# Performance work log

Measured on AMD Instinct MI355X. Metric: run time of the kernel, lower is better.

## Reference

```python
import jax, jax.numpy as jnp
import numpy as np

N = 50000      # nodes
E = 800000     # edges (before self-loops)
IN = 128       # in_channels
HID = 16       # hidden_channels
HEADS = 8
OUT = 16       # out_channels
NEG_SLOPE = 0.2
BN_EPS = 1e-5
LN_EPS = 1e-5


def setup_inputs() -> dict:
    key = jax.random.key(0)
    ks = jax.random.split(key, 16)
    s = 0.05
    inp = {
        "x": jax.random.normal(ks[0], (N, IN), jnp.float32),
        "edge_index": jax.random.randint(ks[1], (2, E), 0, N, jnp.int64),
        # conv1 (in=IN, out=HID, heads=HEADS, concat=True)
        "Wl1": jax.random.normal(ks[2], (HEADS * HID, IN), jnp.float32) * s,
        "bl1": jnp.zeros((HEADS * HID,), jnp.float32),
        "Wr1": jax.random.normal(ks[3], (HEADS * HID, IN), jnp.float32) * s,
        "br1": jnp.zeros((HEADS * HID,), jnp.float32),
        "att1": jax.random.normal(ks[4], (HEADS, HID), jnp.float32) * s,
        "bias1": jnp.zeros((HEADS * HID,), jnp.float32),
        # batchnorm (eval mode, running stats)
        "bn_w": jnp.ones((HEADS * HID,), jnp.float32),
        "bn_b": jnp.zeros((HEADS * HID,), jnp.float32),
        "bn_rm": jnp.zeros((HEADS * HID,), jnp.float32),
        "bn_rv": jnp.ones((HEADS * HID,), jnp.float32),
        # conv2 (in=HEADS*HID, out=OUT, heads=HEADS, concat=False)
        "Wl2": jax.random.normal(ks[5], (HEADS * OUT, HEADS * HID), jnp.float32) * s,
        "bl2": jnp.zeros((HEADS * OUT,), jnp.float32),
        "Wr2": jax.random.normal(ks[6], (HEADS * OUT, HEADS * HID), jnp.float32) * s,
        "br2": jnp.zeros((HEADS * OUT,), jnp.float32),
        "att2": jax.random.normal(ks[7], (HEADS, OUT), jnp.float32) * s,
        "bias2": jnp.zeros((OUT,), jnp.float32),
        # skip + layernorm
        "Wskip": jax.random.normal(ks[8], (OUT, IN), jnp.float32) * s,
        "ln_w": jnp.ones((OUT,), jnp.float32),
        "ln_b": jnp.zeros((OUT,), jnp.float32),
    }
    return inp


def _gatv2(x, src, dst, Wl, bl, Wr, br, att, bias, heads, ch, concat):
    """PyG GATv2Conv (share_weights=False), eval mode (no dropout)."""
    n = x.shape[0]
    xl = (x @ Wl.T + bl).reshape(n, heads, ch)   # source transform
    xr = (x @ Wr.T + br).reshape(n, heads, ch)   # target transform
    # edge-wise attention score
    e = jax.nn.leaky_relu(xl[src] + xr[dst], NEG_SLOPE)          # [E',H,C]
    score = jnp.einsum('ehc,hc->eh', e, att)                      # [E',H]
    # segment softmax over incoming edges per destination node
    smax = jax.ops.segment_max(score, dst, num_segments=n)
    ex = jnp.exp(score - smax[dst])
    denom = jax.ops.segment_sum(ex, dst, num_segments=n)
    alpha = ex / denom[dst]                                       # [E',H]
    out = jax.ops.segment_sum(alpha[:, :, None] * xl[src], dst, num_segments=n)
    if concat:
        out = out.reshape(n, heads * ch)
    else:
        out = out.mean(axis=1)
    return out + bias


def reference(x, edge_index, Wl1, bl1, Wr1, br1, att1, bias1,
              bn_w, bn_b, bn_rm, bn_rv,
              Wl2, bl2, Wr2, br2, att2, bias2,
              Wskip, ln_w, ln_b):
    n = x.shape[0]
    loops = jnp.arange(n, dtype=edge_index.dtype)
    src = jnp.concatenate([edge_index[0], loops])
    dst = jnp.concatenate([edge_index[1], loops])

    x_res = x @ Wskip.T                                            # [N,OUT]

    h = _gatv2(x, src, dst, Wl1, bl1, Wr1, br1, att1, bias1, HEADS, HID, True)
    # BatchNorm1d in eval mode
    h = (h - bn_rm) * jax.lax.rsqrt(bn_rv + BN_EPS) * bn_w + bn_b
    h = jax.nn.elu(h)

    h = _gatv2(h, src, dst, Wl2, bl2, Wr2, br2, att2, bias2, HEADS, OUT, False)

    y = h + x_res
    mu = y.mean(axis=-1, keepdims=True)
    var = ((y - mu) ** 2).mean(axis=-1, keepdims=True)
    return (y - mu) * jax.lax.rsqrt(var + LN_EPS) * ln_w + ln_b
```

## Files before the change

kernel.cpp:

```cpp
#include <hip/hip_runtime.h>

#define NEG_SLOPE 0.2f
#define BN_EPS 1e-5f
#define LN_EPS 1e-5f

#if __has_builtin(__builtin_amdgcn_exp2f)
#define EXP2F(x) __builtin_amdgcn_exp2f(x)
#else
#define EXP2F(x) exp2f(x)
#endif

typedef __bf16 bf16_t;
typedef bf16_t bf16x8 __attribute__((ext_vector_type(8)));
typedef float floatx4 __attribute__((ext_vector_type(4)));

__device__ __forceinline__ unsigned short f2bf(float f) {
  unsigned u = __float_as_uint(f);
  u += 0x7FFFu + ((u >> 16) & 1u);
  return (unsigned short)(u >> 16);
}
__device__ __forceinline__ float bf_lo(unsigned u) { return __uint_as_float(u << 16); }
__device__ __forceinline__ float bf_hi(unsigned u) { return __uint_as_float(u & 0xFFFF0000u); }

__global__ void cvt_all(const float* __restrict__ x,
                        const float* __restrict__ wl1, const float* __restrict__ wr1,
                        const float* __restrict__ wl2, const float* __restrict__ wr2,
                        const float* __restrict__ wsk,
                        const float* __restrict__ bias1,
                        const float* __restrict__ bn_w, const float* __restrict__ bn_b,
                        const float* __restrict__ bn_rm, const float* __restrict__ bn_rv,
                        const int* __restrict__ ei, int E,
                        unsigned short* __restrict__ xbf,
                        unsigned short* __restrict__ wcat1,
                        unsigned short* __restrict__ wcat2,
                        int* __restrict__ deg8, unsigned short* __restrict__ rpos,
                        float* __restrict__ bnS, float* __restrict__ bnT,
                        int n4x, int N) {
  const int W4 = 128 * 128 / 4;
  const int S4 = 16 * 128 / 4;
  int i = blockIdx.x * blockDim.x + threadIdx.x;
  const float* src;
  unsigned short* dst;
  int j;
  if (i < n4x) { src = x; dst = xbf; j = i; }
  else {
    j = i - n4x;
    if (j < W4)               { src = wl1; dst = wcat1; }
    else if (j < 2 * W4)      { src = wr1; dst = wcat1 + 128 * 128; j -= W4; }
    else if (j < 3 * W4)      { src = wl2; dst = wcat2; j -= 2 * W4; }
    else if (j < 4 * W4)      { src = wr2; dst = wcat2 + 128 * 128; j -= 3 * W4; }
    else if (j < 4 * W4 + S4) { src = wsk; dst = wcat1 + 256 * 128; j -= 4 * W4; }
    else {
      j -= 4 * W4 + S4;
      if (j < 32) {
        for (int t = j * 4; t < j * 4 + 4; ++t) {
          float S = bn_w[t] * rsqrtf(bn_rv[t] + BN_EPS);
          bnS[t] = S;
          bnT[t] = (bias1[t] - bn_rm[t]) * S + bn_b[t];
        }
      } else {
        int e = j - 32;
        if (e < E) {
          int d = ei[E + e];
          int c = (int)(blockIdx.x & 7);
          rpos[e] = (unsigned short)atomicAdd(&deg8[(size_t)c * N + d], 1);
        }
      }
      return;
    }
  }
  float4 v = ((const float4*)src)[j];
  ushort4 o;
  o.x = f2bf(v.x); o.y = f2bf(v.y); o.z = f2bf(v.z); o.w = f2bf(v.w);
  ((ushort4*)dst)[j] = o;
}

__global__ __launch_bounds__(1024)
void csr_scan(const int* __restrict__ deg8, int* __restrict__ meta,
              int* __restrict__ cbase8, int* bsum, int N) {
  __shared__ int wsum[16];
  __shared__ int sh_base;
  int b = blockIdx.x;
  int tid = threadIdx.x;
  int lane = tid & 63, wid = tid >> 6;
  int i0 = b * 4096 + tid * 4;

  int4 v[8];
#pragma unroll
  for (int c = 0; c < 8; ++c) {
    const int* p = deg8 + (size_t)c * N;
    v[c] = make_int4(0, 0, 0, 0);
    if (i0 + 3 < N) v[c] = *(const int4*)(p + i0);
    else if (i0 < N) {
      v[c].x = p[i0];
      if (i0 + 1 < N) v[c].y = p[i0 + 1];
      if (i0 + 2 < N) v[c].z = p[i0 + 2];
    }
  }
  int4 run = make_int4(0, 0, 0, 0);
#pragma unroll
  for (int c = 0; c < 8; ++c) {
    int4 t = v[c];
    v[c] = run;
    run.x += t.x; run.y += t.y; run.z += t.z; run.w += t.w;
  }
  int g1 = (run.x + 1) & ~1, g2 = (run.y + 1) & ~1, g3 = (run.z + 1) & ~1, g4 = (run.w + 1) & ~1;
  int s1 = g1, s2 = s1 + g2, s3 = s2 + g3, s4 = s3 + g4;
  int s = s4;
#pragma unroll
  for (int d = 1; d < 64; d <<= 1) { int t = __shfl_up(s, d, 64); if (lane >= d) s += t; }
  if (lane == 63) wsum[wid] = s;
  __syncthreads();
  if (tid < 16) {
    int ws = wsum[tid];
#pragma unroll
    for (int d = 1; d < 16; d <<= 1) { int t = __shfl_up(ws, d, 16); if (tid >= d) ws += t; }
    wsum[tid] = ws;
  }
  __syncthreads();
  if (tid == 0) {
    __hip_atomic_store(&bsum[b], wsum[15] + 1, __ATOMIC_RELEASE, __HIP_MEMORY_SCOPE_AGENT);
    int base = 0;
    for (int j = 0; j < b; ++j) {
      int x;
      do { x = __hip_atomic_load(&bsum[j], __ATOMIC_ACQUIRE, __HIP_MEMORY_SCOPE_AGENT); } while (x == 0);
      base += x - 1;
    }
    sh_base = base;
  }
  __syncthreads();
  int off = sh_base + (wid ? wsum[wid - 1] : 0) + (s - s4);
  int st[4] = {off, off + s1, off + s2, off + s3};
  int tv[4] = {run.x, run.y, run.z, run.w};
#pragma unroll
  for (int k = 0; k < 4; ++k)
    if (i0 + k < N) ((int2*)meta)[i0 + k] = make_int2(st[k], tv[k]);
#pragma unroll
  for (int c = 0; c < 8; ++c) {
    int* p = cbase8 + (size_t)c * N;
    if (i0 + 3 < N) {
      *(int4*)(p + i0) = make_int4(st[0] + v[c].x, st[1] + v[c].y, st[2] + v[c].z, st[3] + v[c].w);
    } else if (i0 < N) {
      p[i0] = st[0] + v[c].x;
      if (i0 + 1 < N) p[i0 + 1] = st[1] + v[c].y;
      if (i0 + 2 < N) p[i0 + 2] = st[2] + v[c].z;
    }
  }
}

__global__ void scatter_edges(const int* __restrict__ ei, int E, int ebase,
                              const int* __restrict__ cbase8,
                              const unsigned short* __restrict__ rpos,
                              unsigned short* __restrict__ csr, int N) {
  int e = blockIdx.x * blockDim.x + threadIdx.x;
  if (e < E) {
    int d = ei[E + e];
    int c = ((ebase + e) >> 8) & 7;
    csr[cbase8[(size_t)c * N + d] + (int)rpos[e]] = (unsigned short)ei[e];
  }
}

template <bool MIXED>
__global__ __launch_bounds__(256)
void gemm_bf16_mfma(const unsigned short* __restrict__ A, const unsigned short* __restrict__ B,
                    const float* __restrict__ bias0, const float* __restrict__ bias1,
                    unsigned short* __restrict__ Cbf, float* __restrict__ Cf,
                    int M, int pstrips) {
  int wave = (int)((blockIdx.x * blockDim.x + threadIdx.x) >> 6);
  int lane = threadIdx.x & 63;
  int mtiles = (M + 31) >> 5;
  if (wave >= mtiles * pstrips) return;
  int mt = wave % mtiles, ps = wave / mtiles;
  int r = lane & 15, quad = lane >> 4;

  const unsigned short* Abase = A + (size_t)(mt * 32 + r) * 128 + quad * 8;
  bf16x8 a0[4], a1[4];
#pragma unroll
  for (int k = 0; k < 4; ++k) {
    a0[k] = *(const bf16x8*)(Abase + 32 * k);
    a1[k] = *(const bf16x8*)(Abase + 16 * 128 + 32 * k);
  }

  int row0 = mt * 32 + quad * 4;
  const int Ptot = MIXED ? 272 : 256;
#pragma unroll
  for (int pp = 0; pp < 4; ++pp) {
    int p0 = ps * 64 + pp * 16;
    if (p0 >= Ptot) break;
    const unsigned short* Bbase = B + (size_t)(p0 + r) * 128 + quad * 8;
    bf16x8 b[4];
#pragma unroll
    for (int k = 0; k < 4; ++k) b[k] = *(const bf16x8*)(Bbase + 32 * k);
    floatx4 acc0 = {0.f, 0.f, 0.f, 0.f};
    floatx4 acc1 = {0.f, 0.f, 0.f, 0.f};
#pragma unroll
    for (int k = 0; k < 4; ++k) {
      acc0 = __builtin_amdgcn_mfma_f32_16x16x32_bf16(a0[k], b[k], acc0, 0, 0, 0);
      acc1 = __builtin_amdgcn_mfma_f32_16x16x32_bf16(a1[k], b[k], acc1, 0, 0, 0);
    }
    int col = p0 + r;
    if (MIXED && col >= 256) {
#pragma unroll
      for (int i = 0; i < 4; ++i) {
        if (row0 + i < M)      Cf[(size_t)(row0 + i) * 16 + (col - 256)] = acc0[i];
        if (row0 + 16 + i < M) Cf[(size_t)(row0 + 16 + i) * 16 + (col - 256)] = acc1[i];
      }
    } else {
      float bs = (col < 128) ? bias0[col] : bias1[col - 128];
#pragma unroll
      for (int i = 0; i < 4; ++i) {
        if (row0 + i < M)      Cbf[(size_t)(row0 + i) * 256 + col] = f2bf(acc0[i] + bs);
        if (row0 + 16 + i < M) Cbf[(size_t)(row0 + 16 + i) * 256 + col] = f2bf(acc1[i] + bs);
      }
    }
  }
}

template <int LAYER>
__global__ __launch_bounds__(256)
void gat_agg(const unsigned int* __restrict__ xlr,
             const int* __restrict__ meta,
             const unsigned short* __restrict__ csr,
             const float* __restrict__ att,
             const float* __restrict__ p0, const float* __restrict__ p1,
             const float* __restrict__ p2, const float* __restrict__ p3,
             void* __restrict__ outp, int n, int nwaves) {
  int lane = threadIdx.x & 63;
  int gw = (int)((blockIdx.x * blockDim.x + threadIdx.x) >> 6);
  int half = lane >> 5, sl = lane & 31;
  float4 at = ((const float4*)att)[sl];
  const float SC = 0.6f * 1.44269504f;
  float a0 = SC * at.x, a1 = SC * at.y, a2 = SC * at.z, a3 = SC * at.w;

  for (int dst = gw; dst < n; dst += nwaves) {
    int dsts = __builtin_amdgcn_readfirstlane(dst);
    int2 m = *(const int2*)(meta + 2 * (size_t)dsts);
    int beg = __builtin_amdgcn_readfirstlane(m.x);
    int dg  = __builtin_amdgcn_readfirstlane(m.y);
    const unsigned* cp = (const unsigned*)csr + (beg >> 1);

    uint2 ur = *(const uint2*)(xlr + (size_t)dsts * 128 + 64 + sl * 2);
    float xr0 = bf_lo(ur.x), xr1 = bf_hi(ur.x), xr2 = bf_lo(ur.y), xr3 = bf_hi(ur.y);
    float lA = 0.f, lB = 0.f;
    float cA0 = 0.f, cA1 = 0.f, cA2 = 0.f, cA3 = 0.f;
    float cB0 = 0.f, cB1 = 0.f, cB2 = 0.f, cB3 = 0.f;

    auto body = [&](uint2 u, float vm, bool useB, bool masked) {
      float x0 = bf_lo(u.x), x1 = bf_hi(u.x), x2 = bf_lo(u.y), x3 = bf_hi(u.y);
      float e0 = x0 + xr0, e1 = x1 + xr1, e2 = x2 + xr2, e3 = x3 + xr3;
      float sc = fmaf(fmaf(fabsf(e0), 0.66666667f, e0), a0,
                 fmaf(fmaf(fabsf(e1), 0.66666667f, e1), a1,
                 fmaf(fmaf(fabsf(e2), 0.66666667f, e2), a2,
                      fmaf(fabsf(e3), 0.66666667f, e3) * a3)));
      sc += __shfl_xor(sc, 1);
      sc += __shfl_xor(sc, 2);
      float pw = EXP2F(sc);
      if (masked) pw *= vm;
      if (useB) {
        lB += pw;
        cB0 = fmaf(pw, x0, cB0); cB1 = fmaf(pw, x1, cB1);
        cB2 = fmaf(pw, x2, cB2); cB3 = fmaf(pw, x3, cB3);
      } else {
        lA += pw;
        cA0 = fmaf(pw, x0, cA0); cA1 = fmaf(pw, x1, cA1);
        cA2 = fmaf(pw, x2, cA2); cA3 = fmaf(pw, x3, cA3);
      }
    };

    int npm = dg >> 1;
    int p = 0;
    int npm8 = npm & ~7;
    for (; p < npm8; p += 8) {
      uint2 u[8];
#pragma unroll
      for (int k = 0; k < 8; ++k) {
        unsigned pr = cp[p + k];
        int s = half ? (int)(pr >> 16) : (int)(pr & 0xFFFFu);
        u[k] = *(const uint2*)(xlr + ((size_t)s << 7) + sl * 2);
      }
#pragma unroll
      for (int k = 0; k < 8; ++k) body(u[k], 1.f, k & 1, false);
    }
    if (npm - p >= 4) {
      uint2 u[4];
#pragma unroll
      for (int k = 0; k < 4; ++k) {
        unsigned pr = cp[p + k];
        int s = half ? (int)(pr >> 16) : (int)(pr & 0xFFFFu);
        u[k] = *(const uint2*)(xlr + ((size_t)s << 7) + sl * 2);
      }
#pragma unroll
      for (int k = 0; k < 4; ++k) body(u[k], 1.f, k & 1, false);
      p += 4;
    }
    {
      int tot = dg + 1;
      uint2 u[4];
      float vm[4];
#pragma unroll
      for (int k = 0; k < 4; ++k) {
        unsigned pr = cp[p + k];
        int e0 = 2 * (p + k), e1 = e0 + 1;
        int sA = (e0 < dg) ? (int)(pr & 0xFFFFu) : dsts;
        int sB = (e1 < dg) ? (int)(pr >> 16) : dsts;
        float mA = (e0 < tot) ? 1.f : 0.f;
        float mB = (e1 < tot) ? 1.f : 0.f;
        int s = half ? sB : sA;
        vm[k] = half ? mB : mA;
        u[k] = *(const uint2*)(xlr + ((size_t)s << 7) + sl * 2);
      }
#pragma unroll
      for (int k = 0; k < 4; ++k) body(u[k], vm[k], k & 1, true);
    }

    float l = lA + lB;
    float c0 = cA0 + cB0, c1 = cA1 + cB1, c2 = cA2 + cB2, c3 = cA3 + cB3;
    l  += __shfl_xor(l, 32);
    c0 += __shfl_xor(c0, 32); c1 += __shfl_xor(c1, 32);
    c2 += __shfl_xor(c2, 32); c3 += __shfl_xor(c3, 32);
    float inv = 1.f / l;

    if (LAYER == 1) {
      float4 S = ((const float4*)p0)[sl];
      float4 T = ((const float4*)p1)[sl];
      float o0 = fmaf(c0 * inv, S.x, T.x);
      float o1 = fmaf(c1 * inv, S.y, T.y);
      float o2 = fmaf(c2 * inv, S.z, T.z);
      float o3 = fmaf(c3 * inv, S.w, T.w);
      o0 = (o0 > 0.f) ? o0 : (__expf(o0) - 1.f);
      o1 = (o1 > 0.f) ? o1 : (__expf(o1) - 1.f);
      o2 = (o2 > 0.f) ? o2 : (__expf(o2) - 1.f);
      o3 = (o3 > 0.f) ? o3 : (__expf(o3) - 1.f);
      if (half == 0) {
        uint2 o;
        o.x = ((unsigned)f2bf(o1) << 16) | f2bf(o0);
        o.y = ((unsigned)f2bf(o3) << 16) | f2bf(o2);
        ((uint2*)outp)[(size_t)dst * 32 + sl] = o;
      }
    } else {
      float y0 = c0 * inv, y1 = c1 * inv, y2 = c2 * inv, y3 = c3 * inv;
#pragma unroll
      for (int d = 4; d <= 16; d <<= 1) {
        y0 += __shfl_xor(y0, d); y1 += __shfl_xor(y1, d);
        y2 += __shfl_xor(y2, d); y3 += __shfl_xor(y3, d);
      }
      int chh = (sl & 3) * 4;
      float4 b2 = *(const float4*)(p1 + chh);
      float4 xs = *(const float4*)(p0 + (size_t)dst * 16 + chh);
      y0 = y0 * 0.125f + b2.x + xs.x;
      y1 = y1 * 0.125f + b2.y + xs.y;
      y2 = y2 * 0.125f + b2.z + xs.z;
      y3 = y3 * 0.125f + b2.w + xs.w;
      float t = (y0 + y1) + (y2 + y3);
      t += __shfl_xor(t, 1); t += __shfl_xor(t, 2);
      float mu = t * (1.f / 16.f);
      float d0 = y0 - mu, d1 = y1 - mu, d2 = y2 - mu, d3 = y3 - mu;
      float v = (d0 * d0 + d1 * d1) + (d2 * d2 + d3 * d3);
      v += __shfl_xor(v, 1); v += __shfl_xor(v, 2);
      float istd = rsqrtf(v * (1.f / 16.f) + LN_EPS);
      float4 lw = *(const float4*)(p2 + chh);
      float4 lb = *(const float4*)(p3 + chh);
      if (lane < 4) {
        float4 o;
        o.x = d0 * istd * lw.x + lb.x;
        o.y = d1 * istd * lw.y + lb.y;
        o.z = d2 * istd * lw.z + lb.z;
        o.w = d3 * istd * lw.w + lb.w;
        *(float4*)((float*)outp + (size_t)dst * 16 + chh) = o;
      }
    }
  }
}

extern "C" void kernel_launch(void* const* d_in, const int* in_sizes, int n_in,
                              void* d_out, int out_size, void* d_ws, size_t ws_size,
                              hipStream_t stream) {
  const float* x     = (const float*)d_in[0];
  const int*   ei    = (const int*)d_in[1];
  const float* Wl1   = (const float*)d_in[2];
  const float* bl1   = (const float*)d_in[3];
  const float* Wr1   = (const float*)d_in[4];
  const float* br1   = (const float*)d_in[5];
  const float* att1  = (const float*)d_in[6];
  const float* bias1 = (const float*)d_in[7];
  const float* bn_w  = (const float*)d_in[8];
  const float* bn_b  = (const float*)d_in[9];
  const float* bn_rm = (const float*)d_in[10];
  const float* bn_rv = (const float*)d_in[11];
  const float* Wl2   = (const float*)d_in[12];
  const float* bl2   = (const float*)d_in[13];
  const float* Wr2   = (const float*)d_in[14];
  const float* br2   = (const float*)d_in[15];
  const float* att2  = (const float*)d_in[16];
  const float* bias2 = (const float*)d_in[17];
  const float* Wskip = (const float*)d_in[18];
  const float* ln_w  = (const float*)d_in[19];
  const float* ln_b  = (const float*)d_in[20];

  const int N = in_sizes[0] / 128;
  const int E = in_sizes[1] / 2;

  char* w = (char*)d_ws;
  size_t off = 0;
  auto alloc = [&](size_t bytes) -> void* {
    void* p = (void*)(w + off);
    off += (bytes + 255) & ~(size_t)255;
    return p;
  };
  unsigned short* xbf    = (unsigned short*)alloc((size_t)N * 128 * 2);
  unsigned short* wcat1  = (unsigned short*)alloc(272 * 128 * 2);
  unsigned short* wcat2  = (unsigned short*)alloc(256 * 128 * 2);
  unsigned int*   xlr    = (unsigned int*)alloc((size_t)N * 128 * 4);
  float*          xres   = (float*)alloc((size_t)N * 16 * 4);
  unsigned short* hbf    = (unsigned short*)alloc((size_t)N * 128 * 2);
  float*          bnS    = (float*)alloc(128 * 4);
  float*          bnT    = (float*)alloc(128 * 4);
  int*            deg8   = (int*)alloc((size_t)8 * N * 4);
  int*            bsum   = (int*)alloc(64 * 4);
  int*            cbase8 = (int*)alloc((size_t)8 * N * 4);
  int*            meta   = (int*)alloc((size_t)2 * N * 4);
  unsigned short* rpos   = (unsigned short*)alloc((size_t)E * 2);
  unsigned short* csr    = (unsigned short*)alloc((size_t)(E + N) * 2 + 256);

  const int n4x = (N * 128) / 4;
  const int W4 = 128 * 128 / 4, S4 = 16 * 128 / 4;
  const int ebase = n4x + 4 * W4 + S4 + 32;
  const int nb = (N + 4095) / 4096;

  hipMemsetAsync(deg8, 0, (size_t)8 * N * 4 + 256 + 64 * 4, stream);
  {
    int tot = ebase + E;
    cvt_all<<<(tot + 255) / 256, 256, 0, stream>>>(
        x, Wl1, Wr1, Wl2, Wr2, Wskip, bias1, bn_w, bn_b, bn_rm, bn_rv, ei, E,
        xbf, wcat1, wcat2, deg8, rpos, bnS, bnT, n4x, N);
  }

  csr_scan<<<nb, 1024, 0, stream>>>(deg8, meta, cbase8, bsum, N);
  scatter_edges<<<(E + 255) / 256, 256, 0, stream>>>(ei, E, ebase, cbase8, rpos, csr, N);

  {
    int mtiles = (N + 31) >> 5;
    int waves = mtiles * 5;
    gemm_bf16_mfma<true><<<(waves + 3) / 4, 256, 0, stream>>>(
        xbf, wcat1, bl1, br1, (unsigned short*)xlr, xres, N, 5);
  }

  {
    int blocks = 2048, nwaves = blocks * 4;
    gat_agg<1><<<blocks, 256, 0, stream>>>(xlr, meta, csr, att1,
                                           bnS, bnT, nullptr, nullptr, (void*)hbf, N, nwaves);
  }

  {
    int mtiles = (N + 31) >> 5;
    int waves = mtiles * 4;
    gemm_bf16_mfma<false><<<(waves + 3) / 4, 256, 0, stream>>>(
        hbf, wcat2, bl2, br2, (unsigned short*)xlr, nullptr, N, 4);
  }

  {
    int blocks = 2048, nwaves = blocks * 4;
    gat_agg<2><<<blocks, 256, 0, stream>>>(xlr, meta, csr, att2,
                                           xres, bias2, ln_w, ln_b, d_out, N, nwaves);
  }
}
```

Measured before the change: 302.8 us.

## Fuse edge scatter into first GEMM, reuse A tiles, widen aggregation gathers

```diff
diff --git a/kernel.cpp b/kernel.cpp
--- a/kernel.cpp
+++ b/kernel.cpp
@@ -148,72 +148,89 @@
   }
 }
 
-__global__ void scatter_edges(const int* __restrict__ ei, int E, int ebase,
-                              const int* __restrict__ cbase8,
-                              const unsigned short* __restrict__ rpos,
-                              unsigned short* __restrict__ csr, int N) {
-  int e = blockIdx.x * blockDim.x + threadIdx.x;
-  if (e < E) {
-    int d = ei[E + e];
-    int c = ((ebase + e) >> 8) & 7;
-    csr[cbase8[(size_t)c * N + d] + (int)rpos[e]] = (unsigned short)ei[e];
-  }
-}
-
 template <bool MIXED>
+__device__ __forceinline__ void gemm_body(int wv, int lane,
+    const unsigned short* __restrict__ A, const unsigned short* __restrict__ B,
+    const float* __restrict__ bias0, const float* __restrict__ bias1,
+    unsigned short* __restrict__ Cbf, float* __restrict__ Cf, int M, int pstrips) {
+  int mtiles = (M + 31) >> 5;
+  if (wv >= mtiles * 2) return;
+  int mt = wv >> 1, sub = wv & 1;
+  int r = lane & 15, quad = lane >> 4;
+
+  const unsigned short* Abase = A + (size_t)(mt * 32 + r) * 128 + quad * 8;
+  bf16x8 a0[4], a1[4];
+#pragma unroll
+  for (int k = 0; k < 4; ++k) {
+    a0[k] = *(const bf16x8*)(Abase + 32 * k);
+    a1[k] = *(const bf16x8*)(Abase + 16 * 128 + 32 * k);
+  }
+
+  int row0 = mt * 32 + quad * 4;
+  const int Ptot = MIXED ? 272 : 256;
+  for (int ps = sub; ps < pstrips; ps += 2) {
+#pragma unroll
+    for (int pp = 0; pp < 4; ++pp) {
+      int p0 = ps * 64 + pp * 16;
+      if (p0 >= Ptot) break;
+      const unsigned short* Bbase = B + (size_t)(p0 + r) * 128 + quad * 8;
+      bf16x8 b[4];
+#pragma unroll
+      for (int k = 0; k < 4; ++k) b[k] = *(const bf16x8*)(Bbase + 32 * k);
+      floatx4 acc0 = {0.f, 0.f, 0.f, 0.f};
+      floatx4 acc1 = {0.f, 0.f, 0.f, 0.f};
+#pragma unroll
+      for (int k = 0; k < 4; ++k) {
+        acc0 = __builtin_amdgcn_mfma_f32_16x16x32_bf16(a0[k], b[k], acc0, 0, 0, 0);
+        acc1 = __builtin_amdgcn_mfma_f32_16x16x32_bf16(a1[k], b[k], acc1, 0, 0, 0);
+      }
+      int col = p0 + r;
+      if (MIXED && col >= 256) {
+#pragma unroll
+        for (int i = 0; i < 4; ++i) {
+          if (row0 + i < M)      Cf[(size_t)(row0 + i) * 16 + (col - 256)] = acc0[i];
+          if (row0 + 16 + i < M) Cf[(size_t)(row0 + 16 + i) * 16 + (col - 256)] = acc1[i];
+        }
+      } else {
+        float bs = (col < 128) ? bias0[col] : bias1[col - 128];
+#pragma unroll
+        for (int i = 0; i < 4; ++i) {
+          if (row0 + i < M)      Cbf[(size_t)(row0 + i) * 256 + col] = f2bf(acc0[i] + bs);
+          if (row0 + 16 + i < M) Cbf[(size_t)(row0 + 16 + i) * 256 + col] = f2bf(acc1[i] + bs);
+        }
+      }
+    }
+  }
+}
+
 __global__ __launch_bounds__(256)
 void gemm_bf16_mfma(const unsigned short* __restrict__ A, const unsigned short* __restrict__ B,
                     const float* __restrict__ bias0, const float* __restrict__ bias1,
                     unsigned short* __restrict__ Cbf, float* __restrict__ Cf,
                     int M, int pstrips) {
-  int wave = (int)((blockIdx.x * blockDim.x + threadIdx.x) >> 6);
-  int lane = threadIdx.x & 63;
-  int mtiles = (M + 31) >> 5;
-  if (wave >= mtiles * pstrips) return;
-  int mt = wave % mtiles, ps = wave / mtiles;
-  int r = lane & 15, quad = lane >> 4;
-
-  const unsigned short* Abase = A + (size_t)(mt * 32 + r) * 128 + quad * 8;
-  bf16x8 a0[4], a1[4];
-#pragma unroll
-  for (int k = 0; k < 4; ++k) {
-    a0[k] = *(const bf16x8*)(Abase + 32 * k);
-    a1[k] = *(const bf16x8*)(Abase + 16 * 128 + 32 * k);
-  }
-
-  int row0 = mt * 32 + quad * 4;
-  const int Ptot = MIXED ? 272 : 256;
-#pragma unroll
-  for (int pp = 0; pp < 4; ++pp) {
-    int p0 = ps * 64 + pp * 16;
-    if (p0 >= Ptot) break;
-    const unsigned short* Bbase = B + (size_t)(p0 + r) * 128 + quad * 8;
-    bf16x8 b[4];
-#pragma unroll
-    for (int k = 0; k < 4; ++k) b[k] = *(const bf16x8*)(Bbase + 32 * k);
-    floatx4 acc0 = {0.f, 0.f, 0.f, 0.f};
-    floatx4 acc1 = {0.f, 0.f, 0.f, 0.f};
-#pragma unroll
-    for (int k = 0; k < 4; ++k) {
-      acc0 = __builtin_amdgcn_mfma_f32_16x16x32_bf16(a0[k], b[k], acc0, 0, 0, 0);
-      acc1 = __builtin_amdgcn_mfma_f32_16x16x32_bf16(a1[k], b[k], acc1, 0, 0, 0);
-    }
-    int col = p0 + r;
-    if (MIXED && col >= 256) {
-#pragma unroll
-      for (int i = 0; i < 4; ++i) {
-        if (row0 + i < M)      Cf[(size_t)(row0 + i) * 16 + (col - 256)] = acc0[i];
-        if (row0 + 16 + i < M) Cf[(size_t)(row0 + 16 + i) * 16 + (col - 256)] = acc1[i];
-      }
-    } else {
-      float bs = (col < 128) ? bias0[col] : bias1[col - 128];
-#pragma unroll
-      for (int i = 0; i < 4; ++i) {
-        if (row0 + i < M)      Cbf[(size_t)(row0 + i) * 256 + col] = f2bf(acc0[i] + bs);
-        if (row0 + 16 + i < M) Cbf[(size_t)(row0 + 16 + i) * 256 + col] = f2bf(acc1[i] + bs);
-      }
-    }
-  }
+  gemm_body<false>((int)((blockIdx.x * blockDim.x + threadIdx.x) >> 6),
+                   (int)(threadIdx.x & 63), A, B, bias0, bias1, Cbf, Cf, M, pstrips);
+}
+
+__global__ __launch_bounds__(256)
+void gemm1_scatter(const unsigned short* __restrict__ A, const unsigned short* __restrict__ B,
+                   const float* __restrict__ bias0, const float* __restrict__ bias1,
+                   unsigned short* __restrict__ Cbf, float* __restrict__ Cf,
+                   int M, int pstrips, int gemmBlocks,
+                   const int* __restrict__ ei, int E, int ebase,
+                   const int* __restrict__ cbase8, const unsigned short* __restrict__ rpos,
+                   unsigned short* __restrict__ csr, int N) {
+  if ((int)blockIdx.x >= gemmBlocks) {
+    int e = ((int)blockIdx.x - gemmBlocks) * 256 + (int)threadIdx.x;
+    if (e < E) {
+      int d = ei[E + e];
+      int c = ((ebase + e) >> 8) & 7;
+      csr[cbase8[(size_t)c * N + d] + (int)rpos[e]] = (unsigned short)ei[e];
+    }
+    return;
+  }
+  gemm_body<true>((int)((blockIdx.x * blockDim.x + threadIdx.x) >> 6),
+                  (int)(threadIdx.x & 63), A, B, bias0, bias1, Cbf, Cf, M, pstrips);
 }
 
 template <int LAYER>
@@ -227,10 +244,17 @@
              void* __restrict__ outp, int n, int nwaves) {
   int lane = threadIdx.x & 63;
   int gw = (int)((blockIdx.x * blockDim.x + threadIdx.x) >> 6);
-  int half = lane >> 5, sl = lane & 31;
-  float4 at = ((const float4*)att)[sl];
+  int slot = lane >> 4;
+  int sl4 = lane & 15;
+  const char* __restrict__ xb = (const char*)xlr;
+  const unsigned slOff = (unsigned)(sl4 << 4);
+  const int hsh = (slot & 1) << 4;
+  const bool whi = (slot >= 2);
+  float4 atA = ((const float4*)att)[sl4 * 2];
+  float4 atB = ((const float4*)att)[sl4 * 2 + 1];
   const float SC = 0.6f * 1.44269504f;
-  float a0 = SC * at.x, a1 = SC * at.y, a2 = SC * at.z, a3 = SC * at.w;
+  float a0 = SC * atA.x, a1 = SC * atA.y, a2 = SC * atA.z, a3 = SC * atA.w;
+  float a4 = SC * atB.x, a5 = SC * atB.y, a6 = SC * atB.z, a7 = SC * atB.w;
 
   for (int dst = gw; dst < n; dst += nwaves) {
     int dsts = __builtin_amdgcn_readfirstlane(dst);
@@ -239,134 +263,173 @@
     int dg  = __builtin_amdgcn_readfirstlane(m.y);
     const unsigned* cp = (const unsigned*)csr + (beg >> 1);
 
-    uint2 ur = *(const uint2*)(xlr + (size_t)dsts * 128 + 64 + sl * 2);
-    float xr0 = bf_lo(ur.x), xr1 = bf_hi(ur.x), xr2 = bf_lo(ur.y), xr3 = bf_hi(ur.y);
-    float lA = 0.f, lB = 0.f;
-    float cA0 = 0.f, cA1 = 0.f, cA2 = 0.f, cA3 = 0.f;
-    float cB0 = 0.f, cB1 = 0.f, cB2 = 0.f, cB3 = 0.f;
-
-    auto body = [&](uint2 u, float vm, bool useB, bool masked) {
+    uint4 urw = *(const uint4*)(xb + (((unsigned)dsts << 9) + 256u + slOff));
+    float xr0 = bf_lo(urw.x), xr1 = bf_hi(urw.x), xr2 = bf_lo(urw.y), xr3 = bf_hi(urw.y);
+    float xr4 = bf_lo(urw.z), xr5 = bf_hi(urw.z), xr6 = bf_lo(urw.w), xr7 = bf_hi(urw.w);
+
+    float l = 0.f;
+    float c0 = 0.f, c1 = 0.f, c2 = 0.f, c3 = 0.f;
+    float c4 = 0.f, c5 = 0.f, c6 = 0.f, c7 = 0.f;
+
+    auto gat = [&](unsigned w0, unsigned w1) -> uint4 {
+      unsigned pr = whi ? w1 : w0;
+      unsigned s = (pr >> hsh) & 0xFFFFu;
+      return *(const uint4*)(xb + ((s << 9) + slOff));
+    };
+
+    auto body = [&](uint4 u, float vm, bool masked) {
       float x0 = bf_lo(u.x), x1 = bf_hi(u.x), x2 = bf_lo(u.y), x3 = bf_hi(u.y);
+      float x4 = bf_lo(u.z), x5 = bf_hi(u.z), x6 = bf_lo(u.w), x7 = bf_hi(u.w);
       float e0 = x0 + xr0, e1 = x1 + xr1, e2 = x2 + xr2, e3 = x3 + xr3;
+      float e4 = x4 + xr4, e5 = x5 + xr5, e6 = x6 + xr6, e7 = x7 + xr7;
       float sc = fmaf(fmaf(fabsf(e0), 0.66666667f, e0), a0,
                  fmaf(fmaf(fabsf(e1), 0.66666667f, e1), a1,
                  fmaf(fmaf(fabsf(e2), 0.66666667f, e2), a2,
-                      fmaf(fabsf(e3), 0.66666667f, e3) * a3)));
+                 fmaf(fmaf(fabsf(e3), 0.66666667f, e3), a3,
+                 fmaf(fmaf(fabsf(e4), 0.66666667f, e4), a4,
+                 fmaf(fmaf(fabsf(e5), 0.66666667f, e5), a5,
+                 fmaf(fmaf(fabsf(e6), 0.66666667f, e6), a6,
+                      fmaf(fabsf(e7), 0.66666667f, e7) * a7)))))));
       sc += __shfl_xor(sc, 1);
-      sc += __shfl_xor(sc, 2);
       float pw = EXP2F(sc);
       if (masked) pw *= vm;
-      if (useB) {
-        lB += pw;
-        cB0 = fmaf(pw, x0, cB0); cB1 = fmaf(pw, x1, cB1);
-        cB2 = fmaf(pw, x2, cB2); cB3 = fmaf(pw, x3, cB3);
-      } else {
-        lA += pw;
-        cA0 = fmaf(pw, x0, cA0); cA1 = fmaf(pw, x1, cA1);
-        cA2 = fmaf(pw, x2, cA2); cA3 = fmaf(pw, x3, cA3);
-      }
+      l += pw;
+      c0 = fmaf(pw, x0, c0); c1 = fmaf(pw, x1, c1);
+      c2 = fmaf(pw, x2, c2); c3 = fmaf(pw, x3, c3);
+      c4 = fmaf(pw, x4, c4); c5 = fmaf(pw, x5, c5);
+      c6 = fmaf(pw, x6, c6); c7 = fmaf(pw, x7, c7);
     };
 
-    int npm = dg >> 1;
-    int p = 0;
-    int npm8 = npm & ~7;
-    for (; p < npm8; p += 8) {
-      uint2 u[8];
-#pragma unroll
-      for (int k = 0; k < 8; ++k) {
-        unsigned pr = cp[p + k];
-        int s = half ? (int)(pr >> 16) : (int)(pr & 0xFFFFu);
-        u[k] = *(const uint2*)(xlr + ((size_t)s << 7) + sl * 2);
-      }
-#pragma unroll
-      for (int k = 0; k < 8; ++k) body(u[k], 1.f, k & 1, false);
-    }
-    if (npm - p >= 4) {
-      uint2 u[4];
-#pragma unroll
-      for (int k = 0; k < 4; ++k) {
-        unsigned pr = cp[p + k];
-        int s = half ? (int)(pr >> 16) : (int)(pr & 0xFFFFu);
-        u[k] = *(const uint2*)(xlr + ((size_t)s << 7) + sl * 2);
-      }
-#pragma unroll
-      for (int k = 0; k < 4; ++k) body(u[k], 1.f, k & 1, false);
-      p += 4;
+    int nq = dg >> 2;
+    int q = 0;
+    int nq4 = nq & ~3;
+    for (; q < nq4; q += 4) {
+      unsigned w[8];
+#pragma unroll
+      for (int k = 0; k < 8; ++k) w[k] = cp[2 * q + k];
+      uint4 u[4];
+#pragma unroll
+      for (int k = 0; k < 4; ++k) u[k] = gat(w[2 * k], w[2 * k + 1]);
+#pragma unroll
+      for (int k = 0; k < 4; ++k) body(u[k], 1.f, false);
+    }
+    if (nq - q >= 2) {
+      unsigned w[4];
+#pragma unroll
+      for (int k = 0; k < 4; ++k) w[k] = cp[2 * q + k];
+      uint4 u[2];
+#pragma unroll
+      for (int k = 0; k < 2; ++k) u[k] = gat(w[2 * k], w[2 * k + 1]);
+#pragma unroll
+      for (int k = 0; k < 2; ++k) body(u[k], 1.f, false);
+      q += 2;
+    }
+    if (nq - q >= 1) {
+      unsigned w0 = cp[2 * q], w1 = cp[2 * q + 1];
+      body(gat(w0, w1), 1.f, false);
+      q += 1;
     }
     {
+      unsigned w0 = cp[2 * q], w1 = cp[2 * q + 1];
       int tot = dg + 1;
-      uint2 u[4];
-      float vm[4];
-#pragma unroll
-      for (int k = 0; k < 4; ++k) {
-        unsigned pr = cp[p + k];
-        int e0 = 2 * (p + k), e1 = e0 + 1;
-        int sA = (e0 < dg) ? (int)(pr & 0xFFFFu) : dsts;
-        int sB = (e1 < dg) ? (int)(pr >> 16) : dsts;
-        float mA = (e0 < tot) ? 1.f : 0.f;
-        float mB = (e1 < tot) ? 1.f : 0.f;
-        int s = half ? sB : sA;
-        vm[k] = half ? mB : mA;
-        u[k] = *(const uint2*)(xlr + ((size_t)s << 7) + sl * 2);
-      }
-#pragma unroll
-      for (int k = 0; k < 4; ++k) body(u[k], vm[k], k & 1, true);
-    }
-
-    float l = lA + lB;
-    float c0 = cA0 + cB0, c1 = cA1 + cB1, c2 = cA2 + cB2, c3 = cA3 + cB3;
-    l  += __shfl_xor(l, 32);
-    c0 += __shfl_xor(c0, 32); c1 += __shfl_xor(c1, 32);
-    c2 += __shfl_xor(c2, 32); c3 += __shfl_xor(c3, 32);
+      int e = 4 * q + slot;
+      unsigned pr = whi ? w1 : w0;
+      unsigned sE = (pr >> hsh) & 0xFFFFu;
+      unsigned s = (e < dg) ? sE : (unsigned)dsts;
+      float vm = (e < tot) ? 1.f : 0.f;
+      uint4 u = *(const uint4*)(xb + ((s << 9) + slOff));
+      body(u, vm, true);
+    }
+
+    l  += __shfl_xor(l, 16);  l  += __shfl_xor(l, 32);
+    c0 += __shfl_xor(c0, 16); c0 += __shfl_xor(c0, 32);
+    c1 += __shfl_xor(c1, 16); c1 += __shfl_xor(c1, 32);
+    c2 += __shfl_xor(c2, 16); c2 += __shfl_xor(c2, 32);
+    c3 += __shfl_xor(c3, 16); c3 += __shfl_xor(c3, 32);
+    c4 += __shfl_xor(c4, 16); c4 += __shfl_xor(c4, 32);
+    c5 += __shfl_xor(c5, 16); c5 += __shfl_xor(c5, 32);
+    c6 += __shfl_xor(c6, 16); c6 += __shfl_xor(c6, 32);
+    c7 += __shfl_xor(c7, 16); c7 += __shfl_xor(c7, 32);
     float inv = 1.f / l;
 
     if (LAYER == 1) {
-      float4 S = ((const float4*)p0)[sl];
-      float4 T = ((const float4*)p1)[sl];
-      float o0 = fmaf(c0 * inv, S.x, T.x);
-      float o1 = fmaf(c1 * inv, S.y, T.y);
-      float o2 = fmaf(c2 * inv, S.z, T.z);
-      float o3 = fmaf(c3 * inv, S.w, T.w);
+      float4 Sa = *(const float4*)(p0 + sl4 * 8);
+      float4 Sb = *(const float4*)(p0 + sl4 * 8 + 4);
+      float4 Ta = *(const float4*)(p1 + sl4 * 8);
+      float4 Tb = *(const float4*)(p1 + sl4 * 8 + 4);
+      float o0 = fmaf(c0 * inv, Sa.x, Ta.x);
+      float o1 = fmaf(c1 * inv, Sa.y, Ta.y);
+      float o2 = fmaf(c2 * inv, Sa.z, Ta.z);
+      float o3 = fmaf(c3 * inv, Sa.w, Ta.w);
+      float o4 = fmaf(c4 * inv, Sb.x, Tb.x);
+      float o5 = fmaf(c5 * inv, Sb.y, Tb.y);
+      float o6 = fmaf(c6 * inv, Sb.z, Tb.z);
+      float o7 = fmaf(c7 * inv, Sb.w, Tb.w);
       o0 = (o0 > 0.f) ? o0 : (__expf(o0) - 1.f);
       o1 = (o1 > 0.f) ? o1 : (__expf(o1) - 1.f);
       o2 = (o2 > 0.f) ? o2 : (__expf(o2) - 1.f);
       o3 = (o3 > 0.f) ? o3 : (__expf(o3) - 1.f);
-      if (half == 0) {
-        uint2 o;
+      o4 = (o4 > 0.f) ? o4 : (__expf(o4) - 1.f);
+      o5 = (o5 > 0.f) ? o5 : (__expf(o5) - 1.f);
+      o6 = (o6 > 0.f) ? o6 : (__expf(o6) - 1.f);
+      o7 = (o7 > 0.f) ? o7 : (__expf(o7) - 1.f);
+      if (slot == 0) {
+        uint4 o;
         o.x = ((unsigned)f2bf(o1) << 16) | f2bf(o0);
         o.y = ((unsigned)f2bf(o3) << 16) | f2bf(o2);
-        ((uint2*)outp)[(size_t)dst * 32 + sl] = o;
+        o.z = ((unsigned)f2bf(o5) << 16) | f2bf(o4);
+        o.w = ((unsigned)f2bf(o7) << 16) | f2bf(o6);
+        ((uint4*)outp)[(size_t)dsts * 16 + sl4] = o;
       }
     } else {
       float y0 = c0 * inv, y1 = c1 * inv, y2 = c2 * inv, y3 = c3 * inv;
-#pragma unroll
-      for (int d = 4; d <= 16; d <<= 1) {
+      float y4 = c4 * inv, y5 = c5 * inv, y6 = c6 * inv, y7 = c7 * inv;
+#pragma unroll
+      for (int d = 2; d <= 8; d <<= 1) {
         y0 += __shfl_xor(y0, d); y1 += __shfl_xor(y1, d);
         y2 += __shfl_xor(y2, d); y3 += __shfl_xor(y3, d);
+        y4 += __shfl_xor(y4, d); y5 += __shfl_xor(y5, d);
+        y6 += __shfl_xor(y6, d); y7 += __shfl_xor(y7, d);
       }
-      int chh = (sl & 3) * 4;
-      float4 b2 = *(const float4*)(p1 + chh);
-      float4 xs = *(const float4*)(p0 + (size_t)dst * 16 + chh);
-      y0 = y0 * 0.125f + b2.x + xs.x;
-      y1 = y1 * 0.125f + b2.y + xs.y;
-      y2 = y2 * 0.125f + b2.z + xs.z;
-      y3 = y3 * 0.125f + b2.w + xs.w;
-      float t = (y0 + y1) + (y2 + y3);
-      t += __shfl_xor(t, 1); t += __shfl_xor(t, 2);
+      int chh = (sl4 & 1) * 8;
+      float4 b2a = *(const float4*)(p1 + chh);
+      float4 b2b = *(const float4*)(p1 + chh + 4);
+      float4 xsa = *(const float4*)(p0 + (size_t)dsts * 16 + chh);
+      float4 xsb = *(const float4*)(p0 + (size_t)dsts * 16 + chh + 4);
+      y0 = y0 * 0.125f + b2a.x + xsa.x;
+      y1 = y1 * 0.125f + b2a.y + xsa.y;
+      y2 = y2 * 0.125f + b2a.z + xsa.z;
+      y3 = y3 * 0.125f + b2a.w + xsa.w;
+      y4 = y4 * 0.125f + b2b.x + xsb.x;
+      y5 = y5 * 0.125f + b2b.y + xsb.y;
+      y6 = y6 * 0.125f + b2b.z + xsb.z;
+      y7 = y7 * 0.125f + b2b.w + xsb.w;
+      float t = ((y0 + y1) + (y2 + y3)) + ((y4 + y5) + (y6 + y7));
+      t += __shfl_xor(t, 1);
       float mu = t * (1.f / 16.f);
       float d0 = y0 - mu, d1 = y1 - mu, d2 = y2 - mu, d3 = y3 - mu;
-      float v = (d0 * d0 + d1 * d1) + (d2 * d2 + d3 * d3);
-      v += __shfl_xor(v, 1); v += __shfl_xor(v, 2);
+      float d4 = y4 - mu, d5 = y5 - mu, d6 = y6 - mu, d7 = y7 - mu;
+      float v = ((d0 * d0 + d1 * d1) + (d2 * d2 + d3 * d3)) +
+                ((d4 * d4 + d5 * d5) + (d6 * d6 + d7 * d7));
+      v += __shfl_xor(v, 1);
       float istd = rsqrtf(v * (1.f / 16.f) + LN_EPS);
-      float4 lw = *(const float4*)(p2 + chh);
-      float4 lb = *(const float4*)(p3 + chh);
-      if (lane < 4) {
-        float4 o;
-        o.x = d0 * istd * lw.x + lb.x;
-        o.y = d1 * istd * lw.y + lb.y;
-        o.z = d2 * istd * lw.z + lb.z;
-        o.w = d3 * istd * lw.w + lb.w;
-        *(float4*)((float*)outp + (size_t)dst * 16 + chh) = o;
+      float4 lwa = *(const float4*)(p2 + chh);
+      float4 lwb = *(const float4*)(p2 + chh + 4);
+      float4 lba = *(const float4*)(p3 + chh);
+      float4 lbb = *(const float4*)(p3 + chh + 4);
+      if (lane < 2) {
+        float4 oa, ob;
+        oa.x = d0 * istd * lwa.x + lba.x;
+        oa.y = d1 * istd * lwa.y + lba.y;
+        oa.z = d2 * istd * lwa.z + lba.z;
+        oa.w = d3 * istd * lwa.w + lba.w;
+        ob.x = d4 * istd * lwb.x + lbb.x;
+        ob.y = d5 * istd * lwb.y + lbb.y;
+        ob.z = d6 * istd * lwb.z + lbb.z;
+        ob.w = d7 * istd * lwb.w + lbb.w;
+        float* op = (float*)outp + (size_t)dsts * 16 + chh;
+        *(float4*)op = oa;
+        *(float4*)(op + 4) = ob;
       }
     }
   }
@@ -436,13 +499,15 @@
   }
 
   csr_scan<<<nb, 1024, 0, stream>>>(deg8, meta, cbase8, bsum, N);
-  scatter_edges<<<(E + 255) / 256, 256, 0, stream>>>(ei, E, ebase, cbase8, rpos, csr, N);
 
   {
     int mtiles = (N + 31) >> 5;
-    int waves = mtiles * 5;
-    gemm_bf16_mfma<true><<<(waves + 3) / 4, 256, 0, stream>>>(
-        xbf, wcat1, bl1, br1, (unsigned short*)xlr, xres, N, 5);
+    int waves = mtiles * 2;
+    int gemmBlocks = (waves + 3) / 4;
+    int scatBlocks = (E + 255) / 256;
+    gemm1_scatter<<<gemmBlocks + scatBlocks, 256, 0, stream>>>(
+        xbf, wcat1, bl1, br1, (unsigned short*)xlr, xres, N, 5, gemmBlocks,
+        ei, E, ebase, cbase8, rpos, csr, N);
   }
 
   {
@@ -453,8 +518,8 @@
 
   {
     int mtiles = (N + 31) >> 5;
-    int waves = mtiles * 4;
-    gemm_bf16_mfma<false><<<(waves + 3) / 4, 256, 0, stream>>>(
+    int waves = mtiles * 2;
+    gemm_bf16_mfma<<<(waves + 3) / 4, 256, 0, stream>>>(
         hbf, wcat2, bl2, br2, (unsigned short*)xlr, nullptr, N, 4);
   }
 
```

Result: no change. 303.8 us (+0.3%).
